# Kernel optimization log

Measured on AMD Instinct MI355X. Metric: run time of the kernel, lower is better.

The kernel has to match this reference:

```python
import jax, jax.numpy as jnp
import numpy as np

N_HEADS = 16


def setup_inputs() -> dict:
    key = jax.random.key(0)
    k1, k2, k3 = jax.random.split(key, 3)
    dim = 1024
    # ragged batch: 16 sequences with lengths 64..1024 (step 64), total_nnz = 8704
    lengths = np.arange(64, 1025, 64, dtype=np.int32)  # (16,)
    cu_seqlens = jnp.asarray(np.concatenate([[0], np.cumsum(lengths)]), dtype=jnp.int32)  # (17,)
    total_nnz = int(lengths.sum())  # 8704
    max_seqlen = int(lengths.max())  # 1024
    hidden_states = jax.random.normal(k1, (total_nnz, dim), dtype=jnp.float32)
    # nn.Linear(dim, 3*dim): weight (3*dim, dim), bias (3*dim)
    Wqkv_weight = jax.random.normal(k2, (3 * dim, dim), dtype=jnp.float32) * (dim ** -0.5)
    Wqkv_bias = jax.random.normal(k3, (3 * dim,), dtype=jnp.float32) * 0.02
    return {
        "hidden_states": hidden_states,
        "Wqkv_weight": Wqkv_weight,
        "Wqkv_bias": Wqkv_bias,
        "cu_seqlens": cu_seqlens,
        "max_seqlen": max_seqlen,
    }


def reference(hidden_states, Wqkv_weight, Wqkv_bias, cu_seqlens, max_seqlen):
    # Unpadded (varlen) self-attention, p_dropout = 0 (eval path).
    nnz, dim = hidden_states.shape
    H = N_HEADS
    D = dim // H
    S = int(max_seqlen)  # static pad length
    B = cu_seqlens.shape[0] - 1

    qkv = hidden_states @ Wqkv_weight.T + Wqkv_bias          # (nnz, 3*dim)
    qkv = qkv.reshape(nnz, 3, H, D)

    seqlens = cu_seqlens[1:] - cu_seqlens[:-1]                # (B,)
    pos = jnp.arange(S)
    valid = pos[None, :] < seqlens[:, None]                   # (B, S) token validity
    gather_idx = jnp.where(valid, cu_seqlens[:-1, None] + pos[None, :], 0)

    qkv_pad = qkv[gather_idx]                                 # (B, S, 3, H, D)
    q = qkv_pad[:, :, 0]                                      # (B, S, H, D)
    k = qkv_pad[:, :, 1]
    v = qkv_pad[:, :, 2]

    scale = 1.0 / jnp.sqrt(jnp.asarray(D, dtype=q.dtype))
    scores = jnp.einsum("bshd,bthd->bhst", q, k) * scale      # (B, H, S, S)
    neg_inf = jnp.asarray(-1e9, dtype=scores.dtype)
    scores = jnp.where(valid[:, None, None, :], scores, neg_inf)  # mask invalid keys
    attn = jax.nn.softmax(scores, axis=-1)
    out_pad = jnp.einsum("bhst,bthd->bshd", attn, v)          # (B, S, H, D)

    # scatter back to unpadded layout (nnz, H*D)
    tok = jnp.arange(nnz)
    tok_b = jnp.searchsorted(cu_seqlens, tok, side="right") - 1
    tok_s = tok - cu_seqlens[tok_b]
    out = out_pad[tok_b, tok_s].reshape(nnz, H * D)
    return out
```

## Files before the change

### kernel.cpp

```cpp
#include <hip/hip_runtime.h>
#include <math.h>


#define HD 64

typedef _Float16 half8 __attribute__((ext_vector_type(8)));
typedef _Float16 half4v __attribute__((ext_vector_type(4)));
typedef float f32x4 __attribute__((ext_vector_type(4)));

#define GLP(p) ((__attribute__((address_space(1))) void*)(p))
#define LDSP(p) ((__attribute__((address_space(3))) void*)(p))

__global__ __launch_bounds__(256)
void cvt_kernel(const float* __restrict__ A, const float* __restrict__ W,
                _Float16* __restrict__ Ah, _Float16* __restrict__ Wh,
                int nA4, int nW4)
{
    int total = nA4 + nW4;
    for (int i = blockIdx.x * blockDim.x + threadIdx.x; i < total;
         i += gridDim.x * blockDim.x) {
        const float* src; _Float16* dst; int j;
        if (i < nA4) { src = A; dst = Ah; j = i; }
        else         { src = W; dst = Wh; j = i - nA4; }
        float4 v = *(const float4*)(src + (size_t)j * 4);
        half4v h;
        h.x = (_Float16)v.x; h.y = (_Float16)v.y;
        h.z = (_Float16)v.z; h.w = (_Float16)v.w;
        *(half4v*)(dst + (size_t)j * 4) = h;
    }
}

__global__ __launch_bounds__(256)
void qkv_gemm_kernel(const _Float16* __restrict__ Ah, const _Float16* __restrict__ Wh,
                     const float* __restrict__ bias,
                     _Float16* __restrict__ Qo, _Float16* __restrict__ Ko,
                     _Float16* __restrict__ Vo,
                     int Kd, int dim)
{
    const int bm = blockIdx.x, bn = blockIdx.y;
    const int t = threadIdx.x;
    const int wid = t >> 6, lane = t & 63;
    const int wr = wid >> 1, wc = wid & 1;
    const int fr = lane & 15, fq = lane >> 4;

    __shared__ _Float16 As[128 * 32];
    __shared__ _Float16 Bs[128 * 32];

    const int m0 = bm * 128, n0 = bn * 128;

    f32x4 acc[4][4];
#pragma unroll
    for (int m = 0; m < 4; ++m)
#pragma unroll
        for (int n = 0; n < 4; ++n) acc[m][n] = (f32x4)0.f;

    float biasv[4];
#pragma unroll
    for (int n = 0; n < 4; ++n)
        biasv[n] = bias[n0 + wc * 64 + n * 16 + fr];

    const int c0 = t, c1 = t + 256;

    for (int k0 = 0; k0 < Kd; k0 += 32) {
        __syncthreads();
        {
            const _Float16* Ab = Ah + (size_t)m0 * Kd + k0;
            const _Float16* Bb = Wh + (size_t)n0 * Kd + k0;
            __builtin_amdgcn_global_load_lds(GLP(Ab + (c0 >> 2) * Kd + (c0 & 3) * 8),
                                             LDSP((char*)As + c0 * 16), 16, 0, 0);
            __builtin_amdgcn_global_load_lds(GLP(Ab + (c1 >> 2) * Kd + (c1 & 3) * 8),
                                             LDSP((char*)As + c1 * 16), 16, 0, 0);
            __builtin_amdgcn_global_load_lds(GLP(Bb + (c0 >> 2) * Kd + (c0 & 3) * 8),
                                             LDSP((char*)Bs + c0 * 16), 16, 0, 0);
            __builtin_amdgcn_global_load_lds(GLP(Bb + (c1 >> 2) * Kd + (c1 & 3) * 8),
                                             LDSP((char*)Bs + c1 * 16), 16, 0, 0);
        }
        __syncthreads();

        half8 a[4], b[4];
#pragma unroll
        for (int m = 0; m < 4; ++m)
            a[m] = *(const half8*)&As[(wr * 64 + m * 16 + fr) * 32 + fq * 8];
#pragma unroll
        for (int n = 0; n < 4; ++n)
            b[n] = *(const half8*)&Bs[(wc * 64 + n * 16 + fr) * 32 + fq * 8];
#pragma unroll
        for (int m = 0; m < 4; ++m)
#pragma unroll
            for (int n = 0; n < 4; ++n)
                acc[m][n] = __builtin_amdgcn_mfma_f32_16x16x32_f16(a[m], b[n], acc[m][n], 0, 0, 0);
    }

    const int which = n0 / dim;
    const int offb  = n0 - which * dim;
    _Float16* dst = (which == 0) ? Qo : (which == 1) ? Ko : Vo;
#pragma unroll
    for (int m = 0; m < 4; ++m) {
#pragma unroll
        for (int n = 0; n < 4; ++n) {
            int gc = offb + wc * 64 + n * 16 + fr;
#pragma unroll
            for (int j = 0; j < 4; ++j) {
                int gm = m0 + wr * 64 + m * 16 + fq * 4 + j;
                dst[(size_t)gm * dim + gc] = (_Float16)(acc[m][n][j] + biasv[n]);
            }
        }
    }
}

__global__ __launch_bounds__(256)
void attn_kernel(const _Float16* __restrict__ Q, const _Float16* __restrict__ K,
                 const _Float16* __restrict__ V, const int* __restrict__ cu,
                 float* __restrict__ out, int dim, int H)
{
    const int bh = blockIdx.x;
    const int b  = bh / H;
    const int h  = bh - b * H;
    const int qt = blockIdx.y;

    const int s0 = cu[b];
    const int L  = cu[b + 1] - s0;
    if (qt * 128 >= L) return;

    const int t    = threadIdx.x;
    const int wid  = t >> 6, lane = t & 63;
    const int fr   = lane & 15, fq = lane >> 4;

    __shared__ _Float16 Ks[64 * 64];
    __shared__ _Float16 Vt[64 * 72];
    __shared__ _Float16 Ps[4][32 * 72];

    _Float16* Psw = &Ps[wid][0];

    half8 aq[2][2];
#pragma unroll
    for (int qm = 0; qm < 2; ++qm)
#pragma unroll
        for (int kc = 0; kc < 2; ++kc) {
            int qrow = qt * 128 + wid * 32 + qm * 16 + fr;
            int qr = (qrow < L) ? qrow : 0;
            half8 v = *(const half8*)(Q + (size_t)(s0 + qr) * dim + h * HD + kc * 32 + fq * 8);
#pragma unroll
            for (int i = 0; i < 8; ++i) v[i] = v[i] * (_Float16)0.125f;
            aq[qm][kc] = v;
        }

    f32x4 o[2][4];
    float m_run[2][4], l_run[2][4];
#pragma unroll
    for (int qm = 0; qm < 2; ++qm) {
#pragma unroll
        for (int n = 0; n < 4; ++n) o[qm][n] = (f32x4)0.f;
#pragma unroll
        for (int j = 0; j < 4; ++j) { m_run[qm][j] = -3.0e38f; l_run[qm][j] = 0.f; }
    }

    const int nkt = (L + 63) >> 6;
    const int vkv = t & 63, vdc = t >> 6;

    for (int kt = 0; kt < nkt; ++kt) {
        __syncthreads();

#pragma unroll
        for (int cc = 0; cc < 2; ++cc) {
            int c    = wid * 2 + cc;
            int phys = c * 1024 + lane * 16;
            int r    = phys >> 7;
            int lb   = (phys & 127) ^ ((r & 7) << 4);
            int krow = kt * 64 + r;
            int kr   = (krow < L) ? krow : 0;
            const char* src = (const char*)K + ((size_t)(s0 + kr) * dim + h * HD) * 2 + lb;
            __builtin_amdgcn_global_load_lds(GLP(src), LDSP((char*)Ks + phys), 16, 0, 0);
        }
        {
            int vrow = kt * 64 + vkv;
            int vr   = (vrow < L) ? vrow : 0;
            const _Float16* sv = V + (size_t)(s0 + vr) * dim + h * HD + vdc * 16;
            half8 v0 = *(const half8*)(sv);
            half8 v1 = *(const half8*)(sv + 8);
#pragma unroll
            for (int i = 0; i < 8; ++i) {
                Vt[(vdc * 16 + i) * 72 + vkv]     = v0[i];
                Vt[(vdc * 16 + 8 + i) * 72 + vkv] = v1[i];
            }
        }
        __syncthreads();

        f32x4 s[2][4];
#pragma unroll
        for (int qm = 0; qm < 2; ++qm)
#pragma unroll
            for (int n = 0; n < 4; ++n) s[qm][n] = (f32x4)0.f;

#pragma unroll
        for (int n = 0; n < 4; ++n)
#pragma unroll
            for (int kc = 0; kc < 2; ++kc) {
                const half8 bk = *(const half8*)((const char*)Ks +
                    ((n * 16 + fr) << 7) + (((kc << 6) + (fq << 4)) ^ ((fr & 7) << 4)));
                s[0][n] = __builtin_amdgcn_mfma_f32_16x16x32_f16(aq[0][kc], bk, s[0][n], 0, 0, 0);
                s[1][n] = __builtin_amdgcn_mfma_f32_16x16x32_f16(aq[1][kc], bk, s[1][n], 0, 0, 0);
            }

        int ksz = L - kt * 64;
        if (ksz < 64) {
#pragma unroll
            for (int n = 0; n < 4; ++n)
                if (n * 16 + fr >= ksz) {
#pragma unroll
                    for (int qm = 0; qm < 2; ++qm)
#pragma unroll
                        for (int j = 0; j < 4; ++j) s[qm][n][j] = -1.0e30f;
                }
        }

#pragma unroll
        for (int qm = 0; qm < 2; ++qm)
#pragma unroll
            for (int j = 0; j < 4; ++j) {
                float mx = fmaxf(fmaxf(s[qm][0][j], s[qm][1][j]),
                                 fmaxf(s[qm][2][j], s[qm][3][j]));
                mx = fmaxf(mx, __shfl_xor(mx, 1));
                mx = fmaxf(mx, __shfl_xor(mx, 2));
                mx = fmaxf(mx, __shfl_xor(mx, 4));
                mx = fmaxf(mx, __shfl_xor(mx, 8));
                float mnew = fmaxf(m_run[qm][j], mx);
                float fac  = __expf(m_run[qm][j] - mnew);
                m_run[qm][j] = mnew;
                float p0 = __expf(s[qm][0][j] - mnew);
                float p1 = __expf(s[qm][1][j] - mnew);
                float p2 = __expf(s[qm][2][j] - mnew);
                float p3 = __expf(s[qm][3][j] - mnew);
                float ls = p0 + p1 + p2 + p3;
                ls += __shfl_xor(ls, 1);
                ls += __shfl_xor(ls, 2);
                ls += __shfl_xor(ls, 4);
                ls += __shfl_xor(ls, 8);
                l_run[qm][j] = l_run[qm][j] * fac + ls;
                o[qm][0][j] *= fac; o[qm][1][j] *= fac;
                o[qm][2][j] *= fac; o[qm][3][j] *= fac;
                int qloc = qm * 16 + fq * 4 + j;
                Psw[qloc * 72 +  0 + fr] = (_Float16)p0;
                Psw[qloc * 72 + 16 + fr] = (_Float16)p1;
                Psw[qloc * 72 + 32 + fr] = (_Float16)p2;
                Psw[qloc * 72 + 48 + fr] = (_Float16)p3;
            }
        __syncthreads();

#pragma unroll
        for (int kc = 0; kc < 2; ++kc) {
            half8 ap0 = *(const half8*)&Psw[(0 * 16 + fr) * 72 + kc * 32 + fq * 8];
            half8 ap1 = *(const half8*)&Psw[(1 * 16 + fr) * 72 + kc * 32 + fq * 8];
#pragma unroll
            for (int n2 = 0; n2 < 4; ++n2) {
                half8 bv = *(const half8*)&Vt[(n2 * 16 + fr) * 72 + kc * 32 + fq * 8];
                o[0][n2] = __builtin_amdgcn_mfma_f32_16x16x32_f16(ap0, bv, o[0][n2], 0, 0, 0);
                o[1][n2] = __builtin_amdgcn_mfma_f32_16x16x32_f16(ap1, bv, o[1][n2], 0, 0, 0);
            }
        }
    }

#pragma unroll
    for (int qm = 0; qm < 2; ++qm)
#pragma unroll
        for (int j = 0; j < 4; ++j) {
            int qrow = qt * 128 + wid * 32 + qm * 16 + fq * 4 + j;
            if (qrow >= L) continue;
            float inv = 1.0f / l_run[qm][j];
#pragma unroll
            for (int n2 = 0; n2 < 4; ++n2)
                out[(size_t)(s0 + qrow) * dim + h * HD + n2 * 16 + fr] = o[qm][n2][j] * inv;
        }
}

extern "C" void kernel_launch(void* const* d_in, const int* in_sizes, int n_in,
                              void* d_out, int out_size, void* d_ws, size_t ws_size,
                              hipStream_t stream)
{
    const float* hs   = (const float*)d_in[0];
    const float* W    = (const float*)d_in[1];
    const float* bias = (const float*)d_in[2];
    const int*   cu   = (const int*)d_in[3];

    const int dim3x = in_sizes[2];
    const int dim   = dim3x / 3;
    const int nnz   = in_sizes[0] / dim;
    const int B     = in_sizes[3] - 1;
    const int H     = dim / HD;
    const size_t nA = (size_t)nnz * dim;
    const size_t nW = (size_t)dim3x * dim;

    _Float16* Ah = (_Float16*)d_ws;
    _Float16* Wh = Ah + nA;
    _Float16* Qh = Wh + nW;
    _Float16* Kh = Qh + nA;
    _Float16* Vh = Kh + nA;

    cvt_kernel<<<1024, 256, 0, stream>>>(hs, W, Ah, Wh, (int)(nA / 4), (int)(nW / 4));

    dim3 g1(nnz / 128, dim3x / 128);
    qkv_gemm_kernel<<<g1, 256, 0, stream>>>(Ah, Wh, bias, Qh, Kh, Vh, dim, dim);

    dim3 g2(B * H, (nnz + 127) / 128);
    attn_kernel<<<g2, 256, 0, stream>>>(Qh, Kh, Vh, cu, (float*)d_out, dim, H);
}
```

Before: 297.4 us.

## Compact attention grid, compute transposed scores, use exp2 softmax with packed V transpose

Replaces the B*H by nnz/128 attention grid, where most blocks exited immediately, with a compact 1D grid. Each block finds its sequence and query tile by scanning cu_seqlens, with longest sequences scheduled first. Scores are computed as K·Q^T so each lane owns one query column. This makes the softmax row reductions mostly in-register with fewer cross-lane shuffles, and the probabilities are written to LDS as vectorised half4 stores. It also folds log2(e) into the Q scale to use exp2, packs the V transpose as paired 32-bit LDS stores, and drops a __syncthreads. In exchange it passes rescale factors through LDS and adds a per-block loop over batch entries.

```diff
diff --git a/kernel.cpp b/kernel.cpp
--- a/kernel.cpp
+++ b/kernel.cpp
@@ -111,16 +111,23 @@
 __global__ __launch_bounds__(256)
 void attn_kernel(const _Float16* __restrict__ Q, const _Float16* __restrict__ K,
                  const _Float16* __restrict__ V, const int* __restrict__ cu,
-                 float* __restrict__ out, int dim, int H)
+                 float* __restrict__ out, int dim, int H, int B)
 {
-    const int bh = blockIdx.x;
-    const int b  = bh / H;
-    const int h  = bh - b * H;
-    const int qt = blockIdx.y;
+    const int w  = blockIdx.x;
+    const int h  = w & (H - 1);
+    const int wq = w / H;
+
+    int b = -1, qt = 0, acc = 0;
+    for (int i = B - 1; i >= 0; --i) {
+        int Li = cu[i + 1] - cu[i];
+        int nq = (Li + 127) >> 7;
+        if (wq >= acc && wq < acc + nq) { b = i; qt = wq - acc; }
+        acc += nq;
+    }
+    if (b < 0) return;
 
     const int s0 = cu[b];
     const int L  = cu[b + 1] - s0;
-    if (qt * 128 >= L) return;
 
     const int t    = threadIdx.x;
     const int wid  = t >> 6, lane = t & 63;
@@ -129,34 +136,36 @@
     __shared__ _Float16 Ks[64 * 64];
     __shared__ _Float16 Vt[64 * 72];
     __shared__ _Float16 Ps[4][32 * 72];
+    __shared__ float    Fs[4][32];
 
     _Float16* Psw = &Ps[wid][0];
-
+    float*    Fsw = &Fs[wid][0];
+
+    const _Float16 qscale = (_Float16)(0.125f * 1.44269504f);
     half8 aq[2][2];
 #pragma unroll
-    for (int qm = 0; qm < 2; ++qm)
+    for (int nt = 0; nt < 2; ++nt)
 #pragma unroll
         for (int kc = 0; kc < 2; ++kc) {
-            int qrow = qt * 128 + wid * 32 + qm * 16 + fr;
+            int qrow = qt * 128 + wid * 32 + nt * 16 + fr;
             int qr = (qrow < L) ? qrow : 0;
             half8 v = *(const half8*)(Q + (size_t)(s0 + qr) * dim + h * HD + kc * 32 + fq * 8);
 #pragma unroll
-            for (int i = 0; i < 8; ++i) v[i] = v[i] * (_Float16)0.125f;
-            aq[qm][kc] = v;
+            for (int i = 0; i < 8; ++i) v[i] = v[i] * qscale;
+            aq[nt][kc] = v;
         }
 
     f32x4 o[2][4];
-    float m_run[2][4], l_run[2][4];
-#pragma unroll
-    for (int qm = 0; qm < 2; ++qm) {
+    float m2[2], l2[2];
+#pragma unroll
+    for (int qm = 0; qm < 2; ++qm)
 #pragma unroll
         for (int n = 0; n < 4; ++n) o[qm][n] = (f32x4)0.f;
-#pragma unroll
-        for (int j = 0; j < 4; ++j) { m_run[qm][j] = -3.0e38f; l_run[qm][j] = 0.f; }
-    }
+    m2[0] = m2[1] = -3.0e38f;
+    l2[0] = l2[1] = 0.f;
 
     const int nkt = (L + 63) >> 6;
-    const int vkv = t & 63, vdc = t >> 6;
+    const int vu = t & 31, vdc = t >> 5;
 
     for (int kt = 0; kt < nkt; ++kt) {
         __syncthreads();
@@ -173,79 +182,90 @@
             __builtin_amdgcn_global_load_lds(GLP(src), LDSP((char*)Ks + phys), 16, 0, 0);
         }
         {
-            int vrow = kt * 64 + vkv;
-            int vr   = (vrow < L) ? vrow : 0;
-            const _Float16* sv = V + (size_t)(s0 + vr) * dim + h * HD + vdc * 16;
-            half8 v0 = *(const half8*)(sv);
-            half8 v1 = *(const half8*)(sv + 8);
+            int k0r = kt * 64 + vu * 2;
+            int r0 = (k0r     < L) ? k0r     : 0;
+            int r1 = (k0r + 1 < L) ? k0r + 1 : 0;
+            half8 v0 = *(const half8*)(V + (size_t)(s0 + r0) * dim + h * HD + vdc * 8);
+            half8 v1 = *(const half8*)(V + (size_t)(s0 + r1) * dim + h * HD + vdc * 8);
 #pragma unroll
             for (int i = 0; i < 8; ++i) {
-                Vt[(vdc * 16 + i) * 72 + vkv]     = v0[i];
-                Vt[(vdc * 16 + 8 + i) * 72 + vkv] = v1[i];
+                union { _Float16 h[2]; unsigned u; } pk;
+                pk.h[0] = v0[i]; pk.h[1] = v1[i];
+                *(unsigned*)&Vt[(vdc * 8 + i) * 72 + vu * 2] = pk.u;
             }
         }
         __syncthreads();
 
-        f32x4 s[2][4];
-#pragma unroll
-        for (int qm = 0; qm < 2; ++qm)
-#pragma unroll
-            for (int n = 0; n < 4; ++n) s[qm][n] = (f32x4)0.f;
-
-#pragma unroll
-        for (int n = 0; n < 4; ++n)
+        f32x4 s2[4][2];
+#pragma unroll
+        for (int mt = 0; mt < 4; ++mt)
+#pragma unroll
+            for (int nt = 0; nt < 2; ++nt) s2[mt][nt] = (f32x4)0.f;
+
+#pragma unroll
+        for (int mt = 0; mt < 4; ++mt)
 #pragma unroll
             for (int kc = 0; kc < 2; ++kc) {
                 const half8 bk = *(const half8*)((const char*)Ks +
-                    ((n * 16 + fr) << 7) + (((kc << 6) + (fq << 4)) ^ ((fr & 7) << 4)));
-                s[0][n] = __builtin_amdgcn_mfma_f32_16x16x32_f16(aq[0][kc], bk, s[0][n], 0, 0, 0);
-                s[1][n] = __builtin_amdgcn_mfma_f32_16x16x32_f16(aq[1][kc], bk, s[1][n], 0, 0, 0);
+                    ((mt * 16 + fr) << 7) + (((kc << 6) + (fq << 4)) ^ ((fr & 7) << 4)));
+                s2[mt][0] = __builtin_amdgcn_mfma_f32_16x16x32_f16(bk, aq[0][kc], s2[mt][0], 0, 0, 0);
+                s2[mt][1] = __builtin_amdgcn_mfma_f32_16x16x32_f16(bk, aq[1][kc], s2[mt][1], 0, 0, 0);
             }
 
         int ksz = L - kt * 64;
         if (ksz < 64) {
 #pragma unroll
-            for (int n = 0; n < 4; ++n)
-                if (n * 16 + fr >= ksz) {
-#pragma unroll
-                    for (int qm = 0; qm < 2; ++qm)
-#pragma unroll
-                        for (int j = 0; j < 4; ++j) s[qm][n][j] = -1.0e30f;
+            for (int mt = 0; mt < 4; ++mt)
+#pragma unroll
+                for (int j = 0; j < 4; ++j)
+                    if (mt * 16 + fq * 4 + j >= ksz) {
+                        s2[mt][0][j] = -1.0e30f;
+                        s2[mt][1][j] = -1.0e30f;
+                    }
+        }
+
+#pragma unroll
+        for (int nt = 0; nt < 2; ++nt) {
+            f32x4 mx4 = s2[0][nt];
+#pragma unroll
+            for (int mt = 1; mt < 4; ++mt) {
+#pragma unroll
+                for (int j = 0; j < 4; ++j) mx4[j] = fmaxf(mx4[j], s2[mt][nt][j]);
+            }
+            float mx = fmaxf(fmaxf(mx4[0], mx4[1]), fmaxf(mx4[2], mx4[3]));
+            mx = fmaxf(mx, __shfl_xor(mx, 16));
+            mx = fmaxf(mx, __shfl_xor(mx, 32));
+            float mnew = fmaxf(m2[nt], mx);
+            float facn = __builtin_exp2f(m2[nt] - mnew);
+            m2[nt] = mnew;
+
+            f32x4 sum4 = (f32x4)0.f;
+#pragma unroll
+            for (int mt = 0; mt < 4; ++mt) {
+                half4v ph;
+#pragma unroll
+                for (int j = 0; j < 4; ++j) {
+                    float p = __builtin_exp2f(s2[mt][nt][j] - mnew);
+                    sum4[j] += p;
+                    ph[j] = (_Float16)p;
                 }
-        }
-
-#pragma unroll
-        for (int qm = 0; qm < 2; ++qm)
-#pragma unroll
-            for (int j = 0; j < 4; ++j) {
-                float mx = fmaxf(fmaxf(s[qm][0][j], s[qm][1][j]),
-                                 fmaxf(s[qm][2][j], s[qm][3][j]));
-                mx = fmaxf(mx, __shfl_xor(mx, 1));
-                mx = fmaxf(mx, __shfl_xor(mx, 2));
-                mx = fmaxf(mx, __shfl_xor(mx, 4));
-                mx = fmaxf(mx, __shfl_xor(mx, 8));
-                float mnew = fmaxf(m_run[qm][j], mx);
-                float fac  = __expf(m_run[qm][j] - mnew);
-                m_run[qm][j] = mnew;
-                float p0 = __expf(s[qm][0][j] - mnew);
-                float p1 = __expf(s[qm][1][j] - mnew);
-                float p2 = __expf(s[qm][2][j] - mnew);
-                float p3 = __expf(s[qm][3][j] - mnew);
-                float ls = p0 + p1 + p2 + p3;
-                ls += __shfl_xor(ls, 1);
-                ls += __shfl_xor(ls, 2);
-                ls += __shfl_xor(ls, 4);
-                ls += __shfl_xor(ls, 8);
-                l_run[qm][j] = l_run[qm][j] * fac + ls;
-                o[qm][0][j] *= fac; o[qm][1][j] *= fac;
-                o[qm][2][j] *= fac; o[qm][3][j] *= fac;
-                int qloc = qm * 16 + fq * 4 + j;
-                Psw[qloc * 72 +  0 + fr] = (_Float16)p0;
-                Psw[qloc * 72 + 16 + fr] = (_Float16)p1;
-                Psw[qloc * 72 + 32 + fr] = (_Float16)p2;
-                Psw[qloc * 72 + 48 + fr] = (_Float16)p3;
-            }
-        __syncthreads();
+                *(half4v*)&Psw[(nt * 16 + fr) * 72 + mt * 16 + fq * 4] = ph;
+            }
+            float ls = (sum4[0] + sum4[1]) + (sum4[2] + sum4[3]);
+            ls += __shfl_xor(ls, 16);
+            ls += __shfl_xor(ls, 32);
+            l2[nt] = l2[nt] * facn + ls;
+            if (fq == 0) Fsw[nt * 16 + fr] = facn;
+        }
+
+#pragma unroll
+        for (int qm = 0; qm < 2; ++qm) {
+            f32x4 fj = *(const f32x4*)&Fsw[qm * 16 + fq * 4];
+#pragma unroll
+            for (int n2 = 0; n2 < 4; ++n2)
+#pragma unroll
+                for (int j = 0; j < 4; ++j) o[qm][n2][j] *= fj[j];
+        }
 
 #pragma unroll
         for (int kc = 0; kc < 2; ++kc) {
@@ -260,17 +280,20 @@
         }
     }
 
-#pragma unroll
-    for (int qm = 0; qm < 2; ++qm)
+    if (fq == 0) { Fsw[fr] = l2[0]; Fsw[16 + fr] = l2[1]; }
+#pragma unroll
+    for (int qm = 0; qm < 2; ++qm) {
+        f32x4 lj = *(const f32x4*)&Fsw[qm * 16 + fq * 4];
 #pragma unroll
         for (int j = 0; j < 4; ++j) {
             int qrow = qt * 128 + wid * 32 + qm * 16 + fq * 4 + j;
             if (qrow >= L) continue;
-            float inv = 1.0f / l_run[qm][j];
+            float inv = 1.0f / lj[j];
 #pragma unroll
             for (int n2 = 0; n2 < 4; ++n2)
                 out[(size_t)(s0 + qrow) * dim + h * HD + n2 * 16 + fr] = o[qm][n2][j] * inv;
         }
+    }
 }
 
 extern "C" void kernel_launch(void* const* d_in, const int* in_sizes, int n_in,
@@ -301,6 +324,6 @@
     dim3 g1(nnz / 128, dim3x / 128);
     qkv_gemm_kernel<<<g1, 256, 0, stream>>>(Ah, Wh, bias, Qh, Kh, Vh, dim, dim);
 
-    dim3 g2(B * H, (nnz + 127) / 128);
-    attn_kernel<<<g2, 256, 0, stream>>>(Qh, Kh, Vh, cu, (float*)d_out, dim, H);
+    const int maxWQ = nnz / 128 + B;
+    attn_kernel<<<maxWQ * H, 256, 0, stream>>>(Qh, Kh, Vh, cu, (float*)d_out, dim, H, B);
 }
```

Result: faster. 259.6 us (-12.7%).
